# Kernel optimization log

Measured on AMD Instinct MI355X. Metric: run time of the kernel, lower is better.

## Reference

```python
import jax, jax.numpy as jnp
import numpy as np

H = 128
M = 50000
L = 400000
EPS = 1e-9


def setup_inputs() -> dict:
    key = jax.random.key(0)
    ks = jax.random.split(key, 24)
    d = {
        'x_emb': jax.random.normal(ks[0], (M, H), jnp.float32),
        'child_h': jax.random.normal(ks[1], (M, H), jnp.float32),
        'child_c': jax.random.normal(ks[2], (M, H), jnp.float32),
        'pair_cand_idx': jax.random.randint(ks[3], (L,), 0, M, jnp.int32),
        'pair_child_idx': jax.random.randint(ks[4], (L,), 0, M, jnp.int32),
    }
    s = 1.0 / np.sqrt(H)
    names = ['Wi_w', 'Ui_w', 'Wf_w', 'Uf_w', 'Wo_w', 'Uo_w', 'Wc_w', 'Uc_w', 'Wa_w', 'Ua_w']
    for i, n in enumerate(names):
        d[n] = jax.random.uniform(ks[5 + i], (H, H), jnp.float32, -s, s)
    for i, n in enumerate(['Wi_b', 'Wf_b', 'Wo_b', 'Wc_b', 'Wa_b']):
        d[n] = jax.random.uniform(ks[15 + i], (H,), jnp.float32, -s, s)
    d['v_w'] = jax.random.uniform(ks[20], (H,), jnp.float32, -s, s)
    return d


def reference(x_emb, child_h, child_c, pair_cand_idx, pair_child_idx,
              Wi_w, Ui_w, Wf_w, Uf_w, Wo_w, Uo_w, Wc_w, Uc_w, Wa_w, Ua_w,
              Wi_b, Wf_b, Wo_b, Wc_b, Wa_b, v_w):
    m = x_emb.shape[0]
    ci, chi = pair_cand_idx, pair_child_idx

    # --- segment attention (torch version runs under no_grad) ---
    Ah = child_h @ Wa_w.T + Wa_b          # [M,H]
    Bx = x_emb @ Ua_w.T                   # [M,H]
    e = jnp.tanh(Ah[chi] + Bx[ci]) @ v_w  # [L]
    seg_max = jax.ops.segment_max(e, ci, num_segments=m)
    x_exp = jnp.exp(e - seg_max[ci])
    seg_sum = jax.ops.segment_sum(x_exp, ci, num_segments=m) + EPS
    attn = x_exp / seg_sum[ci]            # [L]
    h_hat = jax.ops.segment_sum(attn[:, None] * child_h[chi], ci, num_segments=m)  # [M,H]

    # --- tree-LSTM gates ---
    i_j = jax.nn.sigmoid(x_emb @ Wi_w.T + Wi_b + h_hat @ Ui_w.T)
    Wfx = x_emb @ Wf_w.T + Wf_b
    Ufh = child_h @ Uf_w.T
    f_pair = jax.nn.sigmoid(Wfx[ci] + Ufh[chi])                       # [L,H]
    sum_f_c = jax.ops.segment_sum(f_pair * child_c[chi], ci, num_segments=m)
    c_t = jnp.tanh(x_emb @ Wc_w.T + Wc_b + h_hat @ Uc_w.T)
    c = i_j * c_t + sum_f_c
    o_j = jax.nn.sigmoid(x_emb @ Wo_w.T + Wo_b + h_hat @ Uo_w.T)
    h = o_j * jnp.tanh(c)
    return (h, c)
```

## Files before the change

### kernel.cpp

```cpp
#include <hip/hip_runtime.h>
#include <cstdint>
#include <cstddef>

#define H 128
#define PSTRIDE 512

typedef __bf16 v8bf __attribute__((ext_vector_type(8)));
typedef __bf16 v4bf __attribute__((ext_vector_type(4)));
typedef float  v4f  __attribute__((ext_vector_type(4)));

__device__ __forceinline__ float ftanh(float x) {
    return 1.f - 2.f / (1.f + __expf(2.f * x));
}
__device__ __forceinline__ float fsigm(float x) {
    return 1.f / (1.f + __expf(-x));
}

struct MatDesc {
    const __bf16* A;
    int           lda;
    const __bf16* Wb;
    const float*  bias;
    __bf16*       C;
    int           ldc;
};
struct MatBatch { MatDesc m[7]; };
struct WPtrs { const float* w[10]; };

__global__ __launch_bounds__(256) void prep_k(WPtrs wp, __bf16* __restrict__ Wb,
                                              const float* __restrict__ x,
                                              const float* __restrict__ chh,
                                              const float* __restrict__ chc,
                                              __bf16* __restrict__ xe,
                                              __bf16* __restrict__ P,
                                              const int* __restrict__ ci,
                                              int* __restrict__ counts,
                                              int MH4, int L) {
    int tid = blockIdx.x * 256 + threadIdx.x;
    if (tid < 40960) {
        int mat = tid >> 12;
        int off = (tid & 4095) << 2;
        v4f a = *(const v4f*)(wp.w[mat] + off);
        v4bf b;
#pragma unroll
        for (int k = 0; k < 4; ++k) b[k] = (__bf16)a[k];
        *(v4bf*)(Wb + mat * 16384 + off) = b;
        return;
    }
    int i = tid - 40960;
    if (i < MH4) {
        v4f a = ((const v4f*)x)[i];
        v4f b = ((const v4f*)chh)[i];
        v4f c = ((const v4f*)chc)[i];
        v4bf ab, bb, cb;
#pragma unroll
        for (int k = 0; k < 4; ++k) {
            ab[k] = (__bf16)a[k]; bb[k] = (__bf16)b[k]; cb[k] = (__bf16)c[k];
        }
        ((v4bf*)xe)[i] = ab;
        int m = i >> 5;
        int q = (i & 31) << 2;
        __bf16* prow = P + (size_t)m * PSTRIDE + q;
        *(v4bf*)prow = bb;
        *(v4bf*)(prow + H) = cb;
        return;
    }
    int l = i - MH4;
    if (l < L) atomicAdd(&counts[ci[l]], 1);
}

__global__ __launch_bounds__(256) void gemm_batch(MatBatch batch, int M) {
    const MatDesc d = batch.m[blockIdx.y];
    __shared__ __bf16 wlds[H][H + 8];

    for (int t = threadIdx.x; t < 2048; t += 256) {
        int n = t >> 4;
        int k = (t & 15) << 3;
        *(v8bf*)&wlds[n][k] = *(const v8bf*)(d.Wb + n * H + k);
    }
    __syncthreads();

    const int wave = threadIdx.x >> 6;
    const int lane = threadIdx.x & 63;
    const int quad = lane >> 4;
    const int l16  = lane & 15;
    const int r0   = blockIdx.x * 128 + wave * 32;

    v4f acc0[8], acc1[8];
#pragma unroll
    for (int nt = 0; nt < 8; ++nt) {
        acc0[nt] = (v4f){0.f, 0.f, 0.f, 0.f};
        acc1[nt] = (v4f){0.f, 0.f, 0.f, 0.f};
    }

    const __bf16* ar0 = d.A + (size_t)(r0 + l16) * d.lda + quad * 8;
    const __bf16* ar1 = d.A + (size_t)(r0 + 16 + l16) * d.lda + quad * 8;
#pragma unroll
    for (int k0 = 0; k0 < H; k0 += 32) {
        v8bf a0 = *(const v8bf*)(ar0 + k0);
        v8bf a1 = *(const v8bf*)(ar1 + k0);
#pragma unroll
        for (int nt = 0; nt < 8; ++nt) {
            v8bf b = *(const v8bf*)(&wlds[nt * 16 + l16][k0 + quad * 8]);
            acc0[nt] = __builtin_amdgcn_mfma_f32_16x16x32_bf16(a0, b, acc0[nt], 0, 0, 0);
            acc1[nt] = __builtin_amdgcn_mfma_f32_16x16x32_bf16(a1, b, acc1[nt], 0, 0, 0);
        }
    }

#pragma unroll
    for (int nt = 0; nt < 8; ++nt) {
        int n = nt * 16 + l16;
        float bia = d.bias ? d.bias[n] : 0.f;
#pragma unroll
        for (int r = 0; r < 4; ++r) {
            int m0 = r0 + quad * 4 + r;
            int m1 = m0 + 16;
            if (m0 < M) d.C[(size_t)m0 * d.ldc + n] = (__bf16)(acc0[nt][r] + bia);
            if (m1 < M) d.C[(size_t)m1 * d.ldc + n] = (__bf16)(acc1[nt][r] + bia);
        }
    }
}

__global__ __launch_bounds__(256) void edge_score(const int* __restrict__ ci,
                                                  const int* __restrict__ chi,
                                                  const float* __restrict__ vw,
                                                  const __bf16* __restrict__ Bx,
                                                  const __bf16* __restrict__ P,
                                                  float* __restrict__ ex_out, int L) {
    int e = blockIdx.x * 8 + (threadIdx.x >> 5);
    if (e >= L) return;
    const int l32 = threadIdx.x & 31;
    const int h = l32 << 2;
    int m  = ci[e];
    int cj = chi[e];

    v4bf a4 = *(const v4bf*)(P + (cj << 9) + 3 * H + h);
    v4bf b4 = *(const v4bf*)(Bx + (m << 7) + h);
    v4f  vv = *(const v4f*)(vw + h);

    float s = 0.f;
#pragma unroll
    for (int k = 0; k < 4; ++k) s += ftanh((float)a4[k] + (float)b4[k]) * vv[k];
    s += __shfl_xor(s, 1);
    s += __shfl_xor(s, 2);
    s += __shfl_xor(s, 4);
    s += __shfl_xor(s, 8);
    s += __shfl_xor(s, 16);
    if (l32 == 0) ex_out[e] = __expf(s);
}

__global__ __launch_bounds__(1024) void scan_local(const int* __restrict__ counts,
                                                   int* __restrict__ excl,
                                                   int* __restrict__ bsums, int M) {
    __shared__ int s[1024];
    int tid = threadIdx.x;
    int idx = blockIdx.x * 1024 + tid;
    int v = (idx < M) ? counts[idx] : 0;
    s[tid] = v;
    __syncthreads();
    for (int off = 1; off < 1024; off <<= 1) {
        int t = (tid >= off) ? s[tid - off] : 0;
        __syncthreads();
        s[tid] += t;
        __syncthreads();
    }
    if (idx < M) excl[idx] = s[tid] - v;
    if (tid == 1023) bsums[blockIdx.x] = s[1023];
}

__global__ __launch_bounds__(1024) void scan_fused(int* __restrict__ rowptr,
                                                   int* __restrict__ cursor,
                                                   const int* __restrict__ bsums,
                                                   const int* __restrict__ counts,
                                                   int M, int nb) {
    __shared__ int s[1024];
    int t = threadIdx.x, b = blockIdx.x;
    int v = (t < nb) ? bsums[t] : 0;
    s[t] = v;
    __syncthreads();
    for (int off = 1; off < 1024; off <<= 1) {
        int tt = (t >= off) ? s[t - off] : 0;
        __syncthreads();
        s[t] += tt;
        __syncthreads();
    }
    int boff = (b == 0) ? 0 : s[b - 1];
    int idx = b * 1024 + t;
    if (idx < M) {
        int val = rowptr[idx] + boff;
        rowptr[idx] = val;
        cursor[idx] = val;
        if (idx == M - 1) rowptr[M] = val + counts[M - 1];
    }
}

__global__ __launch_bounds__(256) void scatter_k(const int* __restrict__ ci,
                                                 const int* __restrict__ chi,
                                                 const float* __restrict__ ex_e,
                                                 int* __restrict__ cursor,
                                                 int* __restrict__ payload,
                                                 float* __restrict__ exs, int L) {
    int l = blockIdx.x * 256 + threadIdx.x;
    if (l < L) {
        float ex = ex_e[l];
        int c = chi[l];
        int pos = atomicAdd(&cursor[ci[l]], 1);
        payload[pos] = c;
        exs[pos] = ex;
    }
}

__global__ __launch_bounds__(256) void segment_fused(const int* __restrict__ rowptr,
                                                     const int* __restrict__ payload,
                                                     const float* __restrict__ exs,
                                                     const __bf16* __restrict__ Wfx,
                                                     const __bf16* __restrict__ P,
                                                     __bf16* __restrict__ hhat,
                                                     float* __restrict__ sumfc, int M) {
    const int wl   = threadIdx.x & 63;
    const int half = wl & 32;
    const int l32  = wl & 31;
    const int m = blockIdx.x * 8 + (threadIdx.x >> 5);
    if (m >= M) return;
    const int start = rowptr[m];
    const int deg   = rowptr[m + 1] - start;
    const int h = l32 << 2;

    v4bf wf4 = *(const v4bf*)(Wfx + (m << 7) + h);
    float wff[4];
#pragma unroll
    for (int k = 0; k < 4; ++k) wff[k] = (float)wf4[k];

    int   pl0 = (l32 < deg) ? payload[start + l32] : 0;
    int   pl1 = (32 + l32 < deg) ? payload[start + 32 + l32] : 0;
    float ex0 = (l32 < deg) ? exs[start + l32] : 0.f;
    float ex1 = (32 + l32 < deg) ? exs[start + 32 + l32] : 0.f;

    float denom = 0.f;
    float acch[4] = {0.f, 0.f, 0.f, 0.f};
    float accf[4] = {0.f, 0.f, 0.f, 0.f};

    const int jcap = deg < 64 ? deg : 64;
    for (int j = 0; j < jcap; ++j) {
        int   cj = __shfl((j & 32) ? pl1 : pl0, half | (j & 31), 64);
        float ex = __shfl((j & 32) ? ex1 : ex0, half | (j & 31), 64);
        int off = (cj << 9) + h;
        v4bf h4 = *(const v4bf*)(P + off);
        v4bf c4 = *(const v4bf*)(P + off + H);
        v4bf u4 = *(const v4bf*)(P + off + 2 * H);
        denom += ex;
#pragma unroll
        for (int k = 0; k < 4; ++k) {
            acch[k] = fmaf(ex, (float)h4[k], acch[k]);
            accf[k] += fsigm(wff[k] + (float)u4[k]) * (float)c4[k];
        }
    }
    for (int j = 64; j < deg; ++j) {
        int   cj = payload[start + j];
        float ex = exs[start + j];
        int off = (cj << 9) + h;
        v4bf h4 = *(const v4bf*)(P + off);
        v4bf c4 = *(const v4bf*)(P + off + H);
        v4bf u4 = *(const v4bf*)(P + off + 2 * H);
        denom += ex;
#pragma unroll
        for (int k = 0; k < 4; ++k) {
            acch[k] = fmaf(ex, (float)h4[k], acch[k]);
            accf[k] += fsigm(wff[k] + (float)u4[k]) * (float)c4[k];
        }
    }

    float inv = 1.f / (denom + 1e-9f);
    v4bf hb;
    v4f sf;
#pragma unroll
    for (int k = 0; k < 4; ++k) { hb[k] = (__bf16)(acch[k] * inv); sf[k] = accf[k]; }
    *(v4bf*)(hhat + (size_t)m * H + h) = hb;
    *(v4f*)(sumfc + (size_t)m * H + h) = sf;
}

__global__ __launch_bounds__(512) void gemm_final(const __bf16* __restrict__ hhat,
                                                  const __bf16* __restrict__ Ui,
                                                  const __bf16* __restrict__ Uc,
                                                  const __bf16* __restrict__ Uo,
                                                  const __bf16* __restrict__ Xi,
                                                  const __bf16* __restrict__ Xc,
                                                  const __bf16* __restrict__ Xo,
                                                  const float* __restrict__ sumfc,
                                                  float* __restrict__ out, int M, int MH) {
    __shared__ __bf16 wl[3][H][H + 8];

    for (int t = threadIdx.x; t < 6144; t += 512) {
        int w = t >> 11;
        int n = (t >> 4) & 127;
        int k = (t & 15) << 3;
        const __bf16* src = (w == 0) ? Ui : (w == 1) ? Uc : Uo;
        *(v8bf*)&wl[w][n][k] = *(const v8bf*)(src + n * H + k);
    }
    __syncthreads();

    const int wave = threadIdx.x >> 6;
    const int lane = threadIdx.x & 63;
    const int quad = lane >> 4;
    const int l16  = lane & 15;
    const int r0   = blockIdx.x * 128 + wave * 16;

    const __bf16* p0 = hhat + (size_t)(r0 + l16) * H + quad * 8;
    v8bf a0[4];
#pragma unroll
    for (int k0 = 0; k0 < 4; ++k0) a0[k0] = *(const v8bf*)(p0 + k0 * 32);

#pragma unroll
    for (int nt = 0; nt < 8; ++nt) {
        v4f ai0 = (v4f){0.f, 0.f, 0.f, 0.f};
        v4f ac0 = ai0, ao0 = ai0;
#pragma unroll
        for (int k0 = 0; k0 < 4; ++k0) {
            v8bf bi = *(const v8bf*)(&wl[0][nt * 16 + l16][k0 * 32 + quad * 8]);
            v8bf bc = *(const v8bf*)(&wl[1][nt * 16 + l16][k0 * 32 + quad * 8]);
            v8bf bo = *(const v8bf*)(&wl[2][nt * 16 + l16][k0 * 32 + quad * 8]);
            ai0 = __builtin_amdgcn_mfma_f32_16x16x32_bf16(a0[k0], bi, ai0, 0, 0, 0);
            ac0 = __builtin_amdgcn_mfma_f32_16x16x32_bf16(a0[k0], bc, ac0, 0, 0, 0);
            ao0 = __builtin_amdgcn_mfma_f32_16x16x32_bf16(a0[k0], bo, ao0, 0, 0, 0);
        }
        int n = nt * 16 + l16;
#pragma unroll
        for (int r = 0; r < 4; ++r) {
            int m0 = r0 + quad * 4 + r;
            if (m0 < M) {
                size_t idx = (size_t)m0 * H + n;
                float ig = fsigm((float)Xi[idx] + ai0[r]);
                float ct = ftanh((float)Xc[idx] + ac0[r]);
                float og = fsigm((float)Xo[idx] + ao0[r]);
                float c = ig * ct + sumfc[idx];
                out[idx] = og * ftanh(c);
                out[MH + idx] = c;
            }
        }
    }
}

extern "C" void kernel_launch(void* const* d_in, const int* in_sizes, int n_in,
                              void* d_out, int out_size, void* d_ws, size_t ws_size,
                              hipStream_t stream) {
    const float* x_emb   = (const float*)d_in[0];
    const float* child_h = (const float*)d_in[1];
    const float* child_c = (const float*)d_in[2];
    const int*   ci      = (const int*)d_in[3];
    const int*   chi     = (const int*)d_in[4];
    const float* Wi_b = (const float*)d_in[15];
    const float* Wf_b = (const float*)d_in[16];
    const float* Wo_b = (const float*)d_in[17];
    const float* Wc_b = (const float*)d_in[18];
    const float* Wa_b = (const float*)d_in[19];
    const float* vw   = (const float*)d_in[20];

    const int M    = in_sizes[0] / H;
    const int L    = in_sizes[3];
    const int Mpad = (M + 127) & ~127;
    const int MH   = M * H;
    const int MH4  = MH / 4;

    char* p = (char*)d_ws;
    auto alloc = [&](size_t bytes) {
        char* r = p;
        p += (bytes + 255) & ~(size_t)255;
        return (void*)r;
    };
    size_t bfbytes = (size_t)Mpad * H * sizeof(__bf16);
    __bf16* xe16   = (__bf16*)alloc(bfbytes);
    __bf16* P      = (__bf16*)alloc((size_t)Mpad * PSTRIDE * sizeof(__bf16));
    __bf16* hhat16 = (__bf16*)alloc(bfbytes);
    __bf16* Bx16   = (__bf16*)alloc(bfbytes);
    __bf16* Wfx16  = (__bf16*)alloc(bfbytes);
    __bf16* Xi16   = (__bf16*)alloc(bfbytes);
    __bf16* Xc16   = (__bf16*)alloc(bfbytes);
    __bf16* Xo16   = (__bf16*)alloc(bfbytes);
    __bf16* Wb     = (__bf16*)alloc(10 * 16384 * sizeof(__bf16));
    float* sumfc   = (float*)alloc((size_t)MH * 4);
    float* ex_e    = (float*)alloc((size_t)L * 4);
    float* exs     = (float*)alloc((size_t)L * 4);
    int*   payload = (int*)alloc((size_t)L * 4);
    int*   counts  = (int*)alloc((size_t)M * 4);
    int*   rowptr  = (int*)alloc((size_t)(M + 1) * 4);
    int*   cursor  = (int*)alloc((size_t)M * 4);
    int*   bsums   = (int*)alloc(1024 * 4);

    hipMemsetAsync(counts, 0, (size_t)M * 4, stream);

    WPtrs wp;
    for (int k = 0; k < 10; ++k) wp.w[k] = (const float*)d_in[5 + k];
    int prep_items = 40960 + MH4 + L;
    prep_k<<<(prep_items + 255) / 256, 256, 0, stream>>>(wp, Wb, x_emb, child_h, child_c,
                                                         xe16, P, ci, counts, MH4, L);

    const __bf16* Wi = Wb + 0 * 16384;
    const __bf16* Ui = Wb + 1 * 16384;
    const __bf16* Wf = Wb + 2 * 16384;
    const __bf16* Uf = Wb + 3 * 16384;
    const __bf16* Wo = Wb + 4 * 16384;
    const __bf16* Uo = Wb + 5 * 16384;
    const __bf16* Wc = Wb + 6 * 16384;
    const __bf16* Uc = Wb + 7 * 16384;
    const __bf16* Wa = Wb + 8 * 16384;
    const __bf16* Ua = Wb + 9 * 16384;

    MatBatch ba{};
    ba.m[0] = MatDesc{P,    PSTRIDE, Wa, Wa_b,    P + 3 * H, PSTRIDE};
    ba.m[1] = MatDesc{xe16, H,       Ua, nullptr, Bx16,      H};
    ba.m[2] = MatDesc{xe16, H,       Wf, Wf_b,    Wfx16,     H};
    ba.m[3] = MatDesc{P,    PSTRIDE, Uf, nullptr, P + 2 * H, PSTRIDE};
    ba.m[4] = MatDesc{xe16, H,       Wi, Wi_b,    Xi16,      H};
    ba.m[5] = MatDesc{xe16, H,       Wc, Wc_b,    Xc16,      H};
    ba.m[6] = MatDesc{xe16, H,       Wo, Wo_b,    Xo16,      H};
    dim3 gA(Mpad / 128, 7);
    gemm_batch<<<gA, 256, 0, stream>>>(ba, M);

    edge_score<<<(L + 7) / 8, 256, 0, stream>>>(ci, chi, vw, Bx16, P, ex_e, L);

    int nb = (M + 1023) / 1024;
    scan_local<<<nb, 1024, 0, stream>>>(counts, rowptr, bsums, M);
    scan_fused<<<nb, 1024, 0, stream>>>(rowptr, cursor, bsums, counts, M, nb);

    scatter_k<<<(L + 255) / 256, 256, 0, stream>>>(ci, chi, ex_e, cursor, payload, exs, L);

    segment_fused<<<(M + 7) / 8, 256, 0, stream>>>(rowptr, payload, exs, Wfx16, P,
                                                   hhat16, sumfc, M);

    gemm_final<<<Mpad / 128, 512, 0, stream>>>(hhat16, Ui, Uc, Uo, Xi16, Xc16, Xo16,
                                               sumfc, (float*)d_out, M, MH);
}
```

Measured before the change: 417.8 us.

## Fuse edge scoring into scatter, remap gemm_batch blocks, drop LDS weights in gemm_final

The edge score computation now writes its exp value straight into the CSR payload through the cursor atomic, which removes the separate scatter kernel and the ex_e round trip. gemm_batch uses a 1D grid where groups of 8 row tiles run across all 7 matrices together, so that shared A rows stay in cache. gemm_final drops its 3-matrix LDS staging and reads weights from global/L1, with 256 threads each doing 32 rows. This trades LDS traffic for repeated global weight reads and adds edge-level atomics to the scoring pass.

```diff
diff --git a/kernel.cpp b/kernel.cpp
--- a/kernel.cpp
+++ b/kernel.cpp
@@ -69,13 +69,19 @@
     if (l < L) atomicAdd(&counts[ci[l]], 1);
 }
 
-__global__ __launch_bounds__(256) void gemm_batch(MatBatch batch, int M) {
-    const MatDesc d = batch.m[blockIdx.y];
+__global__ __launch_bounds__(256) void gemm_batch(MatBatch batch, int M, int ntile) {
+    const int blk = blockIdx.x;
+    const int g = blk / 56;
+    const int w = blk % 56;
+    const int j = w >> 3;
+    const int t = (g << 3) | (w & 7);
+    if (t >= ntile) return;
+    const MatDesc d = batch.m[j];
     __shared__ __bf16 wlds[H][H + 8];
 
-    for (int t = threadIdx.x; t < 2048; t += 256) {
-        int n = t >> 4;
-        int k = (t & 15) << 3;
+    for (int tt = threadIdx.x; tt < 2048; tt += 256) {
+        int n = tt >> 4;
+        int k = (tt & 15) << 3;
         *(v8bf*)&wlds[n][k] = *(const v8bf*)(d.Wb + n * H + k);
     }
     __syncthreads();
@@ -84,7 +90,7 @@
     const int lane = threadIdx.x & 63;
     const int quad = lane >> 4;
     const int l16  = lane & 15;
-    const int r0   = blockIdx.x * 128 + wave * 32;
+    const int r0   = t * 128 + wave * 32;
 
     v4f acc0[8], acc1[8];
 #pragma unroll
@@ -121,12 +127,14 @@
     }
 }
 
-__global__ __launch_bounds__(256) void edge_score(const int* __restrict__ ci,
-                                                  const int* __restrict__ chi,
-                                                  const float* __restrict__ vw,
-                                                  const __bf16* __restrict__ Bx,
-                                                  const __bf16* __restrict__ P,
-                                                  float* __restrict__ ex_out, int L) {
+__global__ __launch_bounds__(256) void edge_scatter(const int* __restrict__ ci,
+                                                    const int* __restrict__ chi,
+                                                    const float* __restrict__ vw,
+                                                    const __bf16* __restrict__ Bx,
+                                                    const __bf16* __restrict__ P,
+                                                    int* __restrict__ cursor,
+                                                    int* __restrict__ payload,
+                                                    float* __restrict__ exs, int L) {
     int e = blockIdx.x * 8 + (threadIdx.x >> 5);
     if (e >= L) return;
     const int l32 = threadIdx.x & 31;
@@ -146,7 +154,11 @@
     s += __shfl_xor(s, 4);
     s += __shfl_xor(s, 8);
     s += __shfl_xor(s, 16);
-    if (l32 == 0) ex_out[e] = __expf(s);
+    if (l32 == 0) {
+        int pos = atomicAdd(&cursor[m], 1);
+        payload[pos] = cj;
+        exs[pos] = __expf(s);
+    }
 }
 
 __global__ __launch_bounds__(1024) void scan_local(const int* __restrict__ counts,
@@ -194,22 +206,6 @@
     }
 }
 
-__global__ __launch_bounds__(256) void scatter_k(const int* __restrict__ ci,
-                                                 const int* __restrict__ chi,
-                                                 const float* __restrict__ ex_e,
-                                                 int* __restrict__ cursor,
-                                                 int* __restrict__ payload,
-                                                 float* __restrict__ exs, int L) {
-    int l = blockIdx.x * 256 + threadIdx.x;
-    if (l < L) {
-        float ex = ex_e[l];
-        int c = chi[l];
-        int pos = atomicAdd(&cursor[ci[l]], 1);
-        payload[pos] = c;
-        exs[pos] = ex;
-    }
-}
-
 __global__ __launch_bounds__(256) void segment_fused(const int* __restrict__ rowptr,
                                                      const int* __restrict__ payload,
                                                      const float* __restrict__ exs,
@@ -279,7 +275,7 @@
     *(v4f*)(sumfc + (size_t)m * H + h) = sf;
 }
 
-__global__ __launch_bounds__(512) void gemm_final(const __bf16* __restrict__ hhat,
+__global__ __launch_bounds__(256) void gemm_final(const __bf16* __restrict__ hhat,
                                                   const __bf16* __restrict__ Ui,
                                                   const __bf16* __restrict__ Uc,
                                                   const __bf16* __restrict__ Uo,
@@ -288,40 +284,37 @@
                                                   const __bf16* __restrict__ Xo,
                                                   const float* __restrict__ sumfc,
                                                   float* __restrict__ out, int M, int MH) {
-    __shared__ __bf16 wl[3][H][H + 8];
-
-    for (int t = threadIdx.x; t < 6144; t += 512) {
-        int w = t >> 11;
-        int n = (t >> 4) & 127;
-        int k = (t & 15) << 3;
-        const __bf16* src = (w == 0) ? Ui : (w == 1) ? Uc : Uo;
-        *(v8bf*)&wl[w][n][k] = *(const v8bf*)(src + n * H + k);
-    }
-    __syncthreads();
-
     const int wave = threadIdx.x >> 6;
     const int lane = threadIdx.x & 63;
     const int quad = lane >> 4;
     const int l16  = lane & 15;
-    const int r0   = blockIdx.x * 128 + wave * 16;
+    const int r0   = blockIdx.x * 128 + wave * 32;
 
     const __bf16* p0 = hhat + (size_t)(r0 + l16) * H + quad * 8;
-    v8bf a0[4];
-#pragma unroll
-    for (int k0 = 0; k0 < 4; ++k0) a0[k0] = *(const v8bf*)(p0 + k0 * 32);
+    const __bf16* p1 = hhat + (size_t)(r0 + 16 + l16) * H + quad * 8;
+    v8bf a0[4], a1[4];
+#pragma unroll
+    for (int k0 = 0; k0 < 4; ++k0) {
+        a0[k0] = *(const v8bf*)(p0 + k0 * 32);
+        a1[k0] = *(const v8bf*)(p1 + k0 * 32);
+    }
 
 #pragma unroll
     for (int nt = 0; nt < 8; ++nt) {
-        v4f ai0 = (v4f){0.f, 0.f, 0.f, 0.f};
-        v4f ac0 = ai0, ao0 = ai0;
+        const int boff = (nt * 16 + l16) * H + quad * 8;
+        v4f ai0 = (v4f){0.f, 0.f, 0.f, 0.f}, ai1 = ai0;
+        v4f ac0 = ai0, ac1 = ai0, ao0 = ai0, ao1 = ai0;
 #pragma unroll
         for (int k0 = 0; k0 < 4; ++k0) {
-            v8bf bi = *(const v8bf*)(&wl[0][nt * 16 + l16][k0 * 32 + quad * 8]);
-            v8bf bc = *(const v8bf*)(&wl[1][nt * 16 + l16][k0 * 32 + quad * 8]);
-            v8bf bo = *(const v8bf*)(&wl[2][nt * 16 + l16][k0 * 32 + quad * 8]);
+            v8bf bi = *(const v8bf*)(Ui + boff + k0 * 32);
+            v8bf bc = *(const v8bf*)(Uc + boff + k0 * 32);
+            v8bf bo = *(const v8bf*)(Uo + boff + k0 * 32);
             ai0 = __builtin_amdgcn_mfma_f32_16x16x32_bf16(a0[k0], bi, ai0, 0, 0, 0);
+            ai1 = __builtin_amdgcn_mfma_f32_16x16x32_bf16(a1[k0], bi, ai1, 0, 0, 0);
             ac0 = __builtin_amdgcn_mfma_f32_16x16x32_bf16(a0[k0], bc, ac0, 0, 0, 0);
+            ac1 = __builtin_amdgcn_mfma_f32_16x16x32_bf16(a1[k0], bc, ac1, 0, 0, 0);
             ao0 = __builtin_amdgcn_mfma_f32_16x16x32_bf16(a0[k0], bo, ao0, 0, 0, 0);
+            ao1 = __builtin_amdgcn_mfma_f32_16x16x32_bf16(a1[k0], bo, ao1, 0, 0, 0);
         }
         int n = nt * 16 + l16;
 #pragma unroll
@@ -332,6 +325,16 @@
                 float ig = fsigm((float)Xi[idx] + ai0[r]);
                 float ct = ftanh((float)Xc[idx] + ac0[r]);
                 float og = fsigm((float)Xo[idx] + ao0[r]);
+                float c = ig * ct + sumfc[idx];
+                out[idx] = og * ftanh(c);
+                out[MH + idx] = c;
+            }
+            int m1 = m0 + 16;
+            if (m1 < M) {
+                size_t idx = (size_t)m1 * H + n;
+                float ig = fsigm((float)Xi[idx] + ai1[r]);
+                float ct = ftanh((float)Xc[idx] + ac1[r]);
+                float og = fsigm((float)Xo[idx] + ao1[r]);
                 float c = ig * ct + sumfc[idx];
                 out[idx] = og * ftanh(c);
                 out[MH + idx] = c;
@@ -378,7 +381,6 @@
     __bf16* Xo16   = (__bf16*)alloc(bfbytes);
     __bf16* Wb     = (__bf16*)alloc(10 * 16384 * sizeof(__bf16));
     float* sumfc   = (float*)alloc((size_t)MH * 4);
-    float* ex_e    = (float*)alloc((size_t)L * 4);
     float* exs     = (float*)alloc((size_t)L * 4);
     int*   payload = (int*)alloc((size_t)L * 4);
     int*   counts  = (int*)alloc((size_t)M * 4);
@@ -413,20 +415,20 @@
     ba.m[4] = MatDesc{xe16, H,       Wi, Wi_b,    Xi16,      H};
     ba.m[5] = MatDesc{xe16, H,       Wc, Wc_b,    Xc16,      H};
     ba.m[6] = MatDesc{xe16, H,       Wo, Wo_b,    Xo16,      H};
-    dim3 gA(Mpad / 128, 7);
-    gemm_batch<<<gA, 256, 0, stream>>>(ba, M);
-
-    edge_score<<<(L + 7) / 8, 256, 0, stream>>>(ci, chi, vw, Bx16, P, ex_e, L);
+    const int ntile = Mpad / 128;
+    const int ntile8 = (ntile + 7) & ~7;
+    gemm_batch<<<7 * ntile8, 256, 0, stream>>>(ba, M, ntile);
 
     int nb = (M + 1023) / 1024;
     scan_local<<<nb, 1024, 0, stream>>>(counts, rowptr, bsums, M);
     scan_fused<<<nb, 1024, 0, stream>>>(rowptr, cursor, bsums, counts, M, nb);
 
-    scatter_k<<<(L + 255) / 256, 256, 0, stream>>>(ci, chi, ex_e, cursor, payload, exs, L);
+    edge_scatter<<<(L + 7) / 8, 256, 0, stream>>>(ci, chi, vw, Bx16, P, cursor,
+                                                  payload, exs, L);
 
     segment_fused<<<(M + 7) / 8, 256, 0, stream>>>(rowptr, payload, exs, Wfx16, P,
                                                    hhat16, sumfc, M);
 
-    gemm_final<<<Mpad / 128, 512, 0, stream>>>(hhat16, Ui, Uc, Uo, Xi16, Xc16, Xo16,
+    gemm_final<<<Mpad / 128, 256, 0, stream>>>(hhat16, Ui, Uc, Uo, Xi16, Xc16, Xo16,
                                                sumfc, (float*)d_out, M, MH);
 }
```

Result: no change. 412.6 us (-1.3%).
